# Performance work log

Hardware: AMD Instinct MI355X
Metric: run time of the kernel (lower is better)

The kernel has to match this reference:

```python
import jax, jax.numpy as jnp
import numpy as np
from jax import lax

EPS = 1e-5
MIN_SAMPLES = 4
RESHAPE = 14        # edge-map downsample factor
KEEP_FRAC = 0.1     # 1 - quantile(0.9)
KERNEL_FRAC = 0.05  # eval-mode log_kernel

SOBEL_X = jnp.array([[-1., 0., 1.], [-2., 0., 2.], [-1., 0., 1.]], jnp.float32)
SOBEL_Y = jnp.array([[-1., -2., -1.], [0., 0., 0.], [1., 2., 1.]], jnp.float32)


def _dwconv3(x, k):
    C = x.shape[1]
    kern = jnp.broadcast_to(k, (C, 1, 3, 3)).astype(x.dtype)
    return lax.conv_general_dilated(x, kern, (1, 1), 'SAME',
        feature_group_count=C, dimension_numbers=('NCHW', 'OIHW', 'NCHW'))


def _erode3(m):
    k = jnp.ones((1, 1, 3, 3), m.dtype)
    s = lax.conv_general_dilated(m, k, (1, 1), 'SAME',
        dimension_numbers=('NCHW', 'OIHW', 'NCHW'))
    return (s >= 9.0).astype(m.dtype)


def _masked_mean(x, mask, axis=-1):
    m = mask.astype(x.dtype)
    return jnp.sum(x * m, axis=axis) / jnp.maximum(jnp.sum(m, axis=axis), 1.0)


def _ssi_norm(x, mask):
    # scale-shift-invariant normalization: masked median shift, masked MAD scale
    big = jnp.where(mask, x, jnp.inf)
    srt = jnp.sort(big, axis=-1)
    n = jnp.sum(mask, axis=-1)
    idx = jnp.maximum((n - 1) // 2, 0)
    med = jnp.take_along_axis(srt, idx[..., None], axis=-1)
    med = jnp.where(n[..., None] > 0, med, 0.0)
    scale = _masked_mean(jnp.abs(x - med), mask, axis=-1)[..., None]
    return (x - med) / jnp.maximum(scale, EPS)


def _get_edge(image, vmask):
    gx = _dwconv3(image, SOBEL_X) / 8.0
    gy = _dwconv3(image, SOBEL_Y) / 8.0
    gx = jnp.sqrt(jnp.mean(gx * gx, axis=1, keepdims=True))
    gy = jnp.sqrt(jnp.mean(gy * gy, axis=1, keepdims=True))
    edges = jnp.sqrt(gx * gx + gy * gy)
    H, W = edges.shape[-2:]
    bm = jnp.zeros((H, W), edges.dtype).at[3:H - 3, 3:W - 3].set(1.0)
    return edges * bm * vmask


def _resize_bilinear(x, oh, ow):
    # torch F.interpolate bilinear, align_corners=False, no antialias
    B, C, H, W = x.shape
    def coords(o, s):
        c = jnp.clip((jnp.arange(o) + 0.5) * (s / o) - 0.5, 0.0, s - 1.0)
        i0 = jnp.floor(c).astype(jnp.int32)
        return i0, jnp.minimum(i0 + 1, s - 1), c - i0
    y0, y1, wy = coords(oh, H)
    x0, x1, wx = coords(ow, W)
    wy = wy[:, None]; wx = wx[None, :]
    g = lambda yi, xi: x[:, :, yi[:, None], xi[None, :]]
    return (g(y0, x0) * (1 - wy) * (1 - wx) + g(y0, x1) * (1 - wy) * wx
          + g(y1, x0) * wy * (1 - wx) + g(y1, x1) * wy * wx)


def _sample_edges(edges):
    B, _, H, W = edges.shape
    oh, ow = H // RESHAPE, W // RESHAPE
    e = _resize_bilinear(edges, oh, ow).reshape(B, -1)
    k = max(int(KEEP_FRAC * oh * ow), 10)
    _, idx = lax.top_k(e, k)
    return jnp.stack([(idx // ow) * RESHAPE, (idx % ow) * RESHAPE], -1).astype(jnp.int32)


def _extract_patches(x, coords, kh, kw):
    # vectorized irregular patch gather: [B,C,H,W] + [B,P,2] -> [B,P*C,kh*kw]
    B, C, H, W = x.shape
    ph, pw = kh // 2, kw // 2
    xp = jnp.pad(x, ((0, 0), (0, 0), (ph, ph), (pw, pw)))
    dy = jnp.arange(-ph, ph + 1)
    dx = jnp.arange(-pw, pw + 1)
    def one(img, y, x_):
        return img[:, (y + dy)[:, None], (x_ + dx)[None, :]]
    patches = jax.vmap(jax.vmap(one, in_axes=(None, 0, 0)))(
        xp, coords[..., 0] + ph, coords[..., 1] + pw)  # [B,P,C,kh,kw]
    return patches.reshape(B, -1, kh * kw)


def _forward(inp, tgt, mask, image, vmask):
    mask = mask.astype(bool)
    inp = inp.astype(jnp.float32)
    tgt = tgt.astype(jnp.float32)
    B, _, H, W = inp.shape
    vm = _erode3(vmask.astype(jnp.float32))
    edges = _get_edge(image.astype(jnp.float32), vm)
    coords = _sample_edges(edges)
    ks = int(KERNEL_FRAC * min(H, W))
    ks += int(ks % 2 == 0)
    # local patch branch
    pin = _extract_patches(inp, coords, ks, ks)
    ptg = _extract_patches(tgt, coords, ks, ks)
    pmk = _extract_patches(mask.astype(jnp.float32), coords, ks, ks) > 0.5
    pin = _ssi_norm(pin, pmk)
    ptg = _ssi_norm(ptg, pmk)
    err = jnp.maximum(jnp.abs(pin - ptg), EPS)
    valid = jnp.sum(pmk, axis=-1) >= MIN_SAMPLES
    ep = jnp.sqrt(jnp.maximum(_masked_mean(err, pmk, -1), EPS))  # [B,P]
    e_patch = _masked_mean(ep, valid, -1)                         # [B]
    # global image branch
    gi = _ssi_norm(inp.reshape(B, 1, H * W), mask.reshape(B, 1, H * W))
    gt = _ssi_norm(tgt.reshape(B, 1, H * W), mask.reshape(B, 1, H * W))
    gerr = jnp.maximum(jnp.abs(gi - gt), EPS)
    e_glob = jnp.sqrt(jnp.maximum(_masked_mean(gerr, mask.reshape(B, 1, H * W), -1), EPS)).squeeze(-1)
    return 0.5 * (e_patch + e_glob)  # [B]


def setup_inputs() -> dict:
    key = jax.random.key(0)
    k1, k2, k3, k4 = jax.random.split(key, 4)
    B, H, W = 32, 480, 640
    return {
        'input': jax.random.uniform(k1, (B, 1, H, W), jnp.float32, 0.1, 10.0),
        'target': jax.random.uniform(k2, (B, 1, H, W), jnp.float32, 0.1, 10.0),
        'mask': jax.random.bernoulli(k3, 0.9, (B, 1, H, W)),
        'image': jax.random.normal(k4, (B, 3, H, W), jnp.float32),
        'validity_mask': jnp.ones((B, 1, H, W), bool),
    }


def reference(input, target, mask, image, validity_mask):
    return _forward(input, target, mask, image, validity_mask)
```

## Files before the change

### kernel.cpp

```cpp
#include <hip/hip_runtime.h>
#include <math.h>

#define BB 32
#define HH 480
#define WW 640
#define HWN (HH * WW)
#define OH 34
#define OW 45
#define OHW (OH * OW)
#define KTOP 153
#define KS 25
#define PHW 12
#define PATCH (KS * KS)
#define RESHAPE_I 14
#define EPSV 1e-5f

#define TSLICE 10
#define TSW (OHW / TSLICE)

#define NSLICE 16
#define CAP 16384
#define LCAP 2048
#define CPAD 32

__device__ __forceinline__ unsigned int fkey(float f) {
  unsigned int u = __float_as_uint(f);
  return (u & 0x80000000u) ? ~u : (u | 0x80000000u);
}
__device__ __forceinline__ float fkey_inv(unsigned int k) {
  unsigned int u = (k & 0x80000000u) ? (k & 0x7FFFFFFFu) : ~k;
  return __uint_as_float(u);
}

__device__ __forceinline__ float breduce256(float v, float* red) {
  const int t = threadIdx.x;
  __syncthreads();
  red[t] = v;
  __syncthreads();
  for (int s2 = 128; s2 > 0; s2 >>= 1) {
    if (t < s2) red[t] += red[t + s2];
    __syncthreads();
  }
  float r = red[0];
  __syncthreads();
  return r;
}

__device__ __forceinline__ float2 breduce256x2(float a, float b, float* red) {
  const int t = threadIdx.x;
  __syncthreads();
  red[t] = a;
  red[256 + t] = b;
  __syncthreads();
  for (int s2 = 128; s2 > 0; s2 >>= 1) {
    if (t < s2) {
      red[t] += red[t + s2];
      red[256 + t] += red[256 + t + s2];
    }
    __syncthreads();
  }
  float2 r = make_float2(red[0], red[256]);
  __syncthreads();
  return r;
}

__device__ float edge_at(const float* __restrict__ image, const unsigned char* __restrict__ vmask,
                         int b, int y, int x) {
  if (y < 3 || y >= HH - 3 || x < 3 || x >= WW - 3) return 0.f;
  const unsigned char* vm = vmask + (size_t)b * HWN;
  #pragma unroll
  for (int dy = -1; dy <= 1; ++dy) {
    #pragma unroll
    for (int dx = -1; dx <= 1; ++dx) {
      if (!vm[(size_t)(y + dy) * WW + (x + dx)]) return 0.f;
    }
  }
  const float* img = image + (size_t)b * 3 * HWN;
  float sx2 = 0.f, sy2 = 0.f;
  #pragma unroll
  for (int c = 0; c < 3; ++c) {
    const float* p = img + (size_t)c * HWN + (size_t)y * WW + x;
    float a00 = p[-WW - 1], a01 = p[-WW], a02 = p[-WW + 1];
    float a10 = p[-1],                    a12 = p[1];
    float a20 = p[WW - 1],  a21 = p[WW],  a22 = p[WW + 1];
    float gx = (-a00 + a02 + -2.f * a10 + 2.f * a12 + -a20 + a22) / 8.f;
    float gy = (-a00 + -2.f * a01 + -a02 + a20 + 2.f * a21 + a22) / 8.f;
    sx2 += gx * gx;
    sy2 += gy * gy;
  }
  float gxm = sqrtf(sx2 / 3.f);
  float gym = sqrtf(sy2 / 3.f);
  return sqrtf(gxm * gxm + gym * gym);
}

__global__ __launch_bounds__(256) void edge_resize_kernel(const float* __restrict__ image,
                                                          const unsigned char* __restrict__ vmask,
                                                          float* __restrict__ re) {
  int id = blockIdx.x * 256 + threadIdx.x;
  if (id >= BB * OHW) return;
  int b = id / OHW;
  int rem = id % OHW;
  int oy = rem / OW, ox = rem % OW;

  const float ry = (float)((double)HH / (double)OH);
  const float rx = (float)((double)WW / (double)OW);
  float cy = fminf(fmaxf(((float)oy + 0.5f) * ry - 0.5f, 0.f), (float)(HH - 1));
  float cx = fminf(fmaxf(((float)ox + 0.5f) * rx - 0.5f, 0.f), (float)(WW - 1));
  int y0 = (int)floorf(cy);
  int x0 = (int)floorf(cx);
  int y1 = min(y0 + 1, HH - 1);
  int x1 = min(x0 + 1, WW - 1);
  float wy = cy - (float)y0;
  float wx = cx - (float)x0;

  float g00 = edge_at(image, vmask, b, y0, x0);
  float g01 = edge_at(image, vmask, b, y0, x1);
  float g10 = edge_at(image, vmask, b, y1, x0);
  float g11 = edge_at(image, vmask, b, y1, x1);
  re[id] = g00 * (1.f - wy) * (1.f - wx) + g01 * (1.f - wy) * wx +
           g10 * wy * (1.f - wx) + g11 * wy * wx;
}

__global__ __launch_bounds__(256) void topk_rank_kernel(const float* __restrict__ re,
                                                        int* __restrict__ rpart) {
  const int b = blockIdx.x / TSLICE;
  const int sl = blockIdx.x % TSLICE;
  const int t = threadIdx.x;
  __shared__ float e[OHW];
  for (int i = t; i < OHW; i += 256) e[i] = re[b * OHW + i];
  __syncthreads();

  float vi[6];
  int idx[6], cnt[6];
  #pragma unroll
  for (int q = 0; q < 6; ++q) {
    int i = t + q * 256;
    idx[q] = i;
    vi[q] = (i < OHW) ? e[i] : 0.f;
    cnt[q] = 0;
  }
  const int j0 = sl * TSW;
  for (int jj = 0; jj < TSW; ++jj) {
    int j = j0 + jj;
    float u = e[j];
    #pragma unroll
    for (int q = 0; q < 6; ++q) {
      cnt[q] += (u > vi[q]) || (u == vi[q] && j < idx[q]);
    }
  }
  int* rp = rpart + ((size_t)b * TSLICE + sl) * OHW;
  #pragma unroll
  for (int q = 0; q < 6; ++q) {
    if (idx[q] < OHW) rp[idx[q]] = cnt[q];
  }
}

__global__ __launch_bounds__(256) void topk_write_kernel(const int* __restrict__ rpart,
                                                         int* __restrict__ coords) {
  const int b = blockIdx.x;
  const int t = threadIdx.x;
  const int* rp = rpart + (size_t)b * TSLICE * OHW;
  for (int i = t; i < OHW; i += 256) {
    int rank = 0;
    #pragma unroll
    for (int sl = 0; sl < TSLICE; ++sl) rank += rp[sl * OHW + i];
    if (rank < KTOP) {
      coords[(b * KTOP + rank) * 2 + 0] = (i / OW) * RESHAPE_I;
      coords[(b * KTOP + rank) * 2 + 1] = (i % OW) * RESHAPE_I;
    }
  }
}

__global__ __launch_bounds__(256) void patch_kernel(const float* __restrict__ inp,
                                                    const float* __restrict__ tgt,
                                                    const unsigned char* __restrict__ mask,
                                                    const int* __restrict__ coords,
                                                    float* __restrict__ ep, float* __restrict__ val) {
  const int bk = blockIdx.x;
  const int b = bk / KTOP;
  const int t = threadIdx.x;
  __shared__ unsigned int hist[512];
  __shared__ unsigned int scan[512];
  __shared__ float redf[512];
  __shared__ unsigned int sh_pref[2];
  __shared__ int sh_rank[2];

  const int cy = coords[bk * 2 + 0];
  const int cx = coords[bk * 2 + 1];

  float v_in[3], v_tg[3], mk[3];
  unsigned int k_in[3], k_tg[3];
  #pragma unroll
  for (int q = 0; q < 3; ++q) {
    int i = t + q * 256;
    float mkv = 0.f, vi = 0.f, vt = 0.f;
    if (i < PATCH) {
      int dy = i / KS - PHW, dx = i % KS - PHW;
      int y = cy + dy, x = cx + dx;
      if (y >= 0 && y < HH && x >= 0 && x < WW) {
        size_t off = (size_t)b * HWN + (size_t)y * WW + x;
        if (mask[off]) mkv = 1.f;
        vi = inp[off];
        vt = tgt[off];
      }
    }
    v_in[q] = vi; v_tg[q] = vt; mk[q] = mkv;
    k_in[q] = fkey(vi); k_tg[q] = fkey(vt);
  }

  float pn = 0.f;
  #pragma unroll
  for (int q = 0; q < 3; ++q) pn += mk[q];
  float nf = breduce256(pn, redf);
  int n = (int)(nf + 0.5f);
  int r = (n > 0) ? ((n - 1) >> 1) : 0;

  if (t == 0) {
    sh_pref[0] = 0; sh_pref[1] = 0;
    sh_rank[0] = r; sh_rank[1] = r;
  }
  __syncthreads();

  #pragma unroll
  for (int p = 0; p < 4; ++p) {
    const int shift = 24 - 8 * p;
    hist[t] = 0; hist[t + 256] = 0;
    __syncthreads();
    const int r_in = sh_rank[0], r_tg = sh_rank[1];
    const unsigned int pref_in = sh_pref[0], pref_tg = sh_pref[1];
    #pragma unroll
    for (int q = 0; q < 3; ++q) {
      if (mk[q] != 0.f) {
        unsigned int k = k_in[q];
        if (p == 0 || (k >> (shift + 8)) == pref_in)
          atomicAdd(&hist[(k >> shift) & 255u], 1u);
        unsigned int k2 = k_tg[q];
        if (p == 0 || (k2 >> (shift + 8)) == pref_tg)
          atomicAdd(&hist[256 + ((k2 >> shift) & 255u)], 1u);
      }
    }
    __syncthreads();
    scan[t] = hist[t]; scan[t + 256] = hist[t + 256];
    __syncthreads();
    #pragma unroll
    for (int d = 1; d < 256; d <<= 1) {
      unsigned int a = 0, b2 = 0;
      if (t >= d) { a = scan[t - d]; b2 = scan[256 + t - d]; }
      __syncthreads();
      scan[t] += a; scan[256 + t] += b2;
      __syncthreads();
    }
    unsigned int c1 = scan[t], p1 = (t > 0) ? scan[t - 1] : 0;
    if ((unsigned int)r_in >= p1 && (unsigned int)r_in < c1) {
      sh_pref[0] = (pref_in << 8) | (unsigned int)t;
      sh_rank[0] = r_in - (int)p1;
    }
    unsigned int c2 = scan[256 + t], p2 = (t > 0) ? scan[256 + t - 1] : 0;
    if ((unsigned int)r_tg >= p2 && (unsigned int)r_tg < c2) {
      sh_pref[1] = (pref_tg << 8) | (unsigned int)t;
      sh_rank[1] = r_tg - (int)p2;
    }
    __syncthreads();
  }

  float med_i = (n > 0) ? fkey_inv(sh_pref[0]) : 0.f;
  float med_t = (n > 0) ? fkey_inv(sh_pref[1]) : 0.f;

  float pi = 0.f, pt = 0.f;
  #pragma unroll
  for (int q = 0; q < 3; ++q) {
    if (mk[q] != 0.f) {
      pi += fabsf(v_in[q] - med_i);
      pt += fabsf(v_tg[q] - med_t);
    }
  }
  float2 ss = breduce256x2(pi, pt, redf);
  float si = fmaxf(ss.x / fmaxf(nf, 1.f), EPSV);
  float st = fmaxf(ss.y / fmaxf(nf, 1.f), EPSV);

  float pe = 0.f;
  #pragma unroll
  for (int q = 0; q < 3; ++q) {
    if (mk[q] != 0.f) {
      float a = (v_in[q] - med_i) / si;
      float c = (v_tg[q] - med_t) / st;
      pe += fmaxf(fabsf(a - c), EPSV);
    }
  }
  float es = breduce256(pe, redf);
  if (t == 0) {
    ep[bk] = sqrtf(fmaxf(es / fmaxf(nf, 1.f), EPSV));
    val[bk] = (n >= 4) ? 1.f : 0.f;
  }
}

__global__ __launch_bounds__(256) void preduce_kernel(const float* __restrict__ ep,
                                                      const float* __restrict__ val,
                                                      float* __restrict__ e_patch) {
  const int b = blockIdx.x;
  const int t = threadIdx.x;
  __shared__ float red[512];
  float se = 0.f, sv = 0.f;
  for (int i = t; i < KTOP; i += 256) {
    float v = val[b * KTOP + i];
    se += ep[b * KTOP + i] * v;
    sv += v;
  }
  float2 tt = breduce256x2(se, sv, red);
  if (t == 0) e_patch[b] = tt.x / fmaxf(tt.y, 1.f);
}

__global__ __launch_bounds__(256) void gpassA_kernel(const float* __restrict__ inp,
                                                     const float* __restrict__ tgt,
                                                     const unsigned char* __restrict__ mask,
                                                     unsigned int* __restrict__ ghistA) {
  const int b = blockIdx.x / NSLICE;
  const int sl = blockIdx.x % NSLICE;
  const int t = threadIdx.x;
  __shared__ unsigned int hist[512];
  hist[t] = 0; hist[t + 256] = 0;
  __syncthreads();
  const float4* xi4 = (const float4*)(inp + (size_t)b * HWN);
  const float4* xt4 = (const float4*)(tgt + (size_t)b * HWN);
  const unsigned int* m4 = (const unsigned int*)(mask + (size_t)b * HWN);
  const int per4 = (HWN / NSLICE) / 4;
  const int s0 = sl * per4;
  for (int i = s0 + t; i < s0 + per4; i += 256) {
    unsigned int mm = m4[i];
    if (!mm) continue;
    float4 a = xi4[i], c = xt4[i];
    if (mm & 0x000000FFu) { atomicAdd(&hist[fkey(a.x) >> 24], 1u); atomicAdd(&hist[256 + (fkey(c.x) >> 24)], 1u); }
    if (mm & 0x0000FF00u) { atomicAdd(&hist[fkey(a.y) >> 24], 1u); atomicAdd(&hist[256 + (fkey(c.y) >> 24)], 1u); }
    if (mm & 0x00FF0000u) { atomicAdd(&hist[fkey(a.z) >> 24], 1u); atomicAdd(&hist[256 + (fkey(c.z) >> 24)], 1u); }
    if (mm & 0xFF000000u) { atomicAdd(&hist[fkey(a.w) >> 24], 1u); atomicAdd(&hist[256 + (fkey(c.w) >> 24)], 1u); }
  }
  __syncthreads();
  unsigned int h0 = hist[t], h1 = hist[t + 256];
  if (h0) atomicAdd(&ghistA[(b * 2 + 0) * 256 + t], h0);
  if (h1) atomicAdd(&ghistA[(b * 2 + 1) * 256 + t], h1);
}

__global__ __launch_bounds__(64) void gselA_kernel(const unsigned int* __restrict__ ghistA,
                                                   int* __restrict__ selA) {
  const int bs = blockIdx.x;
  if (threadIdx.x != 0) return;
  const unsigned int* gh = ghistA + bs * 256;
  unsigned int n = 0;
  for (int i = 0; i < 256; ++i) n += gh[i];
  int c1 = -1, r1 = 0;
  unsigned int nb = 0;
  if (n > 0) {
    unsigned int r = (n - 1) >> 1, cum = 0;
    int bin = 0;
    for (; bin < 256; ++bin) {
      unsigned int h = gh[bin];
      if (cum + h > r) break;
      cum += h;
    }
    c1 = bin; r1 = (int)(r - cum); nb = cum;
  }
  selA[bs * 4 + 0] = c1;
  selA[bs * 4 + 1] = r1;
  selA[bs * 4 + 2] = (int)n;
  selA[bs * 4 + 3] = (int)nb;
}

__global__ __launch_bounds__(256) void gpassB_kernel(const float* __restrict__ inp,
                                                     const float* __restrict__ tgt,
                                                     const unsigned char* __restrict__ mask,
                                                     const int* __restrict__ selA,
                                                     unsigned int* __restrict__ ghistB) {
  const int b = blockIdx.x / NSLICE;
  const int sl = blockIdx.x % NSLICE;
  const int t = threadIdx.x;
  __shared__ unsigned int hist[512];
  hist[t] = 0; hist[t + 256] = 0;
  __syncthreads();
  const unsigned int c1i = (unsigned int)selA[(b * 2 + 0) * 4];
  const unsigned int c1t = (unsigned int)selA[(b * 2 + 1) * 4];
  const float4* xi4 = (const float4*)(inp + (size_t)b * HWN);
  const float4* xt4 = (const float4*)(tgt + (size_t)b * HWN);
  const unsigned int* m4 = (const unsigned int*)(mask + (size_t)b * HWN);
  const int per4 = (HWN / NSLICE) / 4;
  const int s0 = sl * per4;
  for (int i = s0 + t; i < s0 + per4; i += 256) {
    unsigned int mm = m4[i];
    if (!mm) continue;
    float4 a = xi4[i], c = xt4[i];
    #define GPB(av, cv, bit) \
      if (mm & bit) { \
        unsigned int k = fkey(av); \
        if ((k >> 24) == c1i) atomicAdd(&hist[(k >> 16) & 255u], 1u); \
        unsigned int k2 = fkey(cv); \
        if ((k2 >> 24) == c1t) atomicAdd(&hist[256 + ((k2 >> 16) & 255u)], 1u); \
      }
    GPB(a.x, c.x, 0x000000FFu)
    GPB(a.y, c.y, 0x0000FF00u)
    GPB(a.z, c.z, 0x00FF0000u)
    GPB(a.w, c.w, 0xFF000000u)
    #undef GPB
  }
  __syncthreads();
  unsigned int h0 = hist[t], h1 = hist[t + 256];
  if (h0) atomicAdd(&ghistB[(b * 2 + 0) * 256 + t], h0);
  if (h1) atomicAdd(&ghistB[(b * 2 + 1) * 256 + t], h1);
}

__global__ __launch_bounds__(64) void gselB_kernel(const unsigned int* __restrict__ ghistB,
                                                   const int* __restrict__ selA,
                                                   int* __restrict__ selB) {
  const int bs = blockIdx.x;
  if (threadIdx.x != 0) return;
  const int c1 = selA[bs * 4 + 0];
  const int r1 = selA[bs * 4 + 1];
  const int n = selA[bs * 4 + 2];
  const int nb1 = selA[bs * 4 + 3];
  if (c1 < 0) {
    selB[bs * 4 + 0] = -1;
    selB[bs * 4 + 1] = 0;
    selB[bs * 4 + 2] = 0;
    selB[bs * 4 + 3] = 0;
    return;
  }
  const unsigned int* gh = ghistB + bs * 256;
  unsigned int r = (unsigned int)r1, cum = 0;
  int bin = 0;
  for (; bin < 256; ++bin) {
    unsigned int h = gh[bin];
    if (cum + h > r) break;
    cum += h;
  }
  selB[bs * 4 + 0] = (c1 << 8) | bin;
  selB[bs * 4 + 1] = (int)(r - cum);
  selB[bs * 4 + 2] = n;
  selB[bs * 4 + 3] = nb1 + (int)cum;
}

__global__ __launch_bounds__(256) void gcollect_kernel(const float* __restrict__ inp,
                                                       const float* __restrict__ tgt,
                                                       const unsigned char* __restrict__ mask,
                                                       const int* __restrict__ selB,
                                                       float* __restrict__ cand,
                                                       unsigned int* __restrict__ ccount,
                                                       float* __restrict__ sbelow,
                                                       float* __restrict__ sabove) {
  const int bs = blockIdx.x / NSLICE;
  const int sl = blockIdx.x % NSLICE;
  const int b = bs >> 1, s = bs & 1;
  const float* x = (s == 0 ? inp : tgt) + (size_t)b * HWN;
  const unsigned char* m = mask + (size_t)b * HWN;
  const int prefix = selB[bs * 4 + 0];
  __shared__ float red[512];
  __shared__ float buf[LCAP];
  __shared__ unsigned int lcnt, gbase;
  const int t = threadIdx.x;
  if (t == 0) lcnt = 0;
  __syncthreads();
  float sb = 0.f, sa = 0.f;
  if (prefix >= 0) {
    float* cd = cand + (size_t)bs * CAP;
    const float4* x4 = (const float4*)x;
    const unsigned int* m4 = (const unsigned int*)m;
    const int per4 = (HWN / NSLICE) / 4;
    const int s0 = sl * per4;
    for (int i = s0 + t; i < s0 + per4; i += 256) {
      unsigned int mm = m4[i];
      if (!mm) continue;
      float4 a = x4[i];
      #define GCOL(av, bit) \
        if (mm & bit) { \
          float v = av; \
          int pf = (int)(fkey(v) >> 16); \
          if (pf < prefix) sb += v; \
          else if (pf > prefix) sa += v; \
          else { \
            unsigned int pos = atomicAdd(&lcnt, 1u); \
            if (pos < LCAP) buf[pos] = v; \
            else { \
              unsigned int g = atomicAdd(&ccount[bs * CPAD], 1u); \
              if (g < CAP) cd[g] = v; \
            } \
          } \
        }
      GCOL(a.x, 0x000000FFu)
      GCOL(a.y, 0x0000FF00u)
      GCOL(a.z, 0x00FF0000u)
      GCOL(a.w, 0xFF000000u)
      #undef GCOL
    }
  }
  __syncthreads();
  if (prefix >= 0) {
    unsigned int c = min(lcnt, (unsigned int)LCAP);
    if (t == 0 && c > 0) gbase = atomicAdd(&ccount[bs * CPAD], c);
    __syncthreads();
    if (c > 0) {
      float* cd = cand + (size_t)bs * CAP;
      unsigned int base = gbase;
      for (unsigned int i = t; i < c; i += 256) {
        unsigned int pos = base + i;
        if (pos < CAP) cd[pos] = buf[i];
      }
    }
  }
  float2 ts = breduce256x2(sb, sa, red);
  if (t == 0) {
    atomicAdd(&sbelow[bs], ts.x);
    atomicAdd(&sabove[bs], ts.y);
  }
}

__global__ __launch_bounds__(256) void gfinal_kernel(const float* __restrict__ cand,
                                                     const unsigned int* __restrict__ ccount,
                                                     const int* __restrict__ selB,
                                                     const float* __restrict__ sbelow,
                                                     const float* __restrict__ sabove,
                                                     float* __restrict__ gstats,
                                                     float* __restrict__ nvals) {
  const int bs = blockIdx.x;
  const int t = threadIdx.x;
  const int prefix = selB[bs * 4 + 0];
  const int r2 = selB[bs * 4 + 1];
  const int n = selB[bs * 4 + 2];
  const int nbelow = selB[bs * 4 + 3];
  __shared__ unsigned int hist[256];
  __shared__ float red[256];
  __shared__ int sh_bin1, sh_r3;
  const float* cd = cand + (size_t)bs * CAP;
  int c = (int)min(ccount[bs * CPAD], (unsigned int)CAP);
  if (prefix < 0) {
    if (t == 0) {
      gstats[bs * 2 + 0] = 0.f;
      gstats[bs * 2 + 1] = 0.f;
      if ((bs & 1) == 0) nvals[bs >> 1] = 0.f;
    }
    return;
  }

  hist[t] = 0;
  __syncthreads();
  for (int i = t; i < c; i += 256)
    atomicAdd(&hist[(fkey(cd[i]) >> 8) & 255u], 1u);
  __syncthreads();
  if (t == 0) {
    unsigned int rr = (unsigned int)r2, cum = 0;
    int bin = 0;
    for (; bin < 256; ++bin) {
      unsigned int h = hist[bin];
      if (cum + h > rr) break;
      cum += h;
    }
    sh_bin1 = bin;
    sh_r3 = (int)(rr - cum);
  }
  __syncthreads();
  const int bin1 = sh_bin1;
  const int r3 = sh_r3;

  hist[t] = 0;
  __syncthreads();
  for (int i = t; i < c; i += 256) {
    unsigned int key = fkey(cd[i]);
    if (((key >> 8) & 255u) == (unsigned int)bin1)
      atomicAdd(&hist[key & 255u], 1u);
  }
  __syncthreads();
  __shared__ float sh_med;
  if (t == 0) {
    unsigned int rr = (unsigned int)r3, cum = 0;
    int bin = 0;
    for (; bin < 256; ++bin) {
      unsigned int h = hist[bin];
      if (cum + h > rr) break;
      cum += h;
    }
    unsigned int key = ((unsigned int)prefix << 16) |
                       ((unsigned int)bin1 << 8) | (unsigned int)bin;
    sh_med = fkey_inv(key);
  }
  __syncthreads();
  const float med = sh_med;

  float ps = 0.f;
  for (int i = t; i < c; i += 256) ps += fabsf(cd[i] - med);
  float scand = breduce256(ps, red);
  if (t == 0) {
    float nb = (float)nbelow;
    float na = (float)(n - nbelow - c);
    float num = (nb * med - sbelow[bs]) + (sabove[bs] - na * med) + scand;
    gstats[bs * 2 + 0] = med;
    gstats[bs * 2 + 1] = num / fmaxf((float)n, 1.f);
    if ((bs & 1) == 0) nvals[bs >> 1] = (float)n;
  }
}

__global__ __launch_bounds__(256) void gerr_kernel(const float* __restrict__ inp,
                                                   const float* __restrict__ tgt,
                                                   const unsigned char* __restrict__ mask,
                                                   const float* __restrict__ gstats,
                                                   float* __restrict__ gacc) {
  const int b = blockIdx.x / NSLICE;
  const int sl = blockIdx.x % NSLICE;
  __shared__ float red[256];
  const int t = threadIdx.x;
  const float med_i = gstats[(b * 2 + 0) * 2 + 0];
  const float sc_i = fmaxf(gstats[(b * 2 + 0) * 2 + 1], EPSV);
  const float med_t = gstats[(b * 2 + 1) * 2 + 0];
  const float sc_t = fmaxf(gstats[(b * 2 + 1) * 2 + 1], EPSV);
  const float ri = 1.f / sc_i, rt = 1.f / sc_t;
  const float4* xi4 = (const float4*)(inp + (size_t)b * HWN);
  const float4* xt4 = (const float4*)(tgt + (size_t)b * HWN);
  const unsigned int* m4 = (const unsigned int*)(mask + (size_t)b * HWN);
  const int per4 = (HWN / NSLICE) / 4;
  const int s0 = sl * per4;
  float part = 0.f;
  for (int i = s0 + t; i < s0 + per4; i += 256) {
    unsigned int mm = m4[i];
    if (!mm) continue;
    float4 a = xi4[i], c = xt4[i];
    if (mm & 0x000000FFu) part += fmaxf(fabsf((a.x - med_i) * ri - (c.x - med_t) * rt), EPSV);
    if (mm & 0x0000FF00u) part += fmaxf(fabsf((a.y - med_i) * ri - (c.y - med_t) * rt), EPSV);
    if (mm & 0x00FF0000u) part += fmaxf(fabsf((a.z - med_i) * ri - (c.z - med_t) * rt), EPSV);
    if (mm & 0xFF000000u) part += fmaxf(fabsf((a.w - med_i) * ri - (c.w - med_t) * rt), EPSV);
  }
  float tp = breduce256(part, red);
  if (t == 0) atomicAdd(&gacc[b], tp);
}

__global__ __launch_bounds__(64) void final_kernel(const float* __restrict__ gacc,
                                                   const float* __restrict__ nvals,
                                                   const float* __restrict__ e_patch,
                                                   float* __restrict__ out) {
  const int b = threadIdx.x;
  if (b < BB) {
    float n = nvals[b];
    float eg = sqrtf(fmaxf(gacc[b] / fmaxf(n, 1.f), EPSV));
    out[b] = 0.5f * (e_patch[b] + eg);
  }
}

extern "C" void kernel_launch(void* const* d_in, const int* in_sizes, int n_in,
                              void* d_out, int out_size, void* d_ws, size_t ws_size,
                              hipStream_t stream) {
  const float* inp = (const float*)d_in[0];
  const float* tgt = (const float*)d_in[1];
  const unsigned char* mask = (const unsigned char*)d_in[2];
  const float* image = (const float*)d_in[3];
  const unsigned char* vmask = (const unsigned char*)d_in[4];
  float* out = (float*)d_out;

  float* ws = (float*)d_ws;
  float* re = ws;
  int* coords = (int*)(ws + 48960);
  float* ep = ws + 48960 + 9792;
  float* val = ep + 4896;
  float* e_patch = val + 4896;
  float* gstats = e_patch + 32;
  float* nvals = gstats + 128;
  int* selA = (int*)(nvals + 32);
  int* selB = selA + 256;
  float* cand = (float*)(selB + 256);
  unsigned int* ghistA = (unsigned int*)(cand + (size_t)64 * CAP);
  unsigned int* ghistB = ghistA + 64 * 256;
  unsigned int* ccount = ghistB + 64 * 256;
  float* sbelow = (float*)(ccount + 64 * CPAD);
  float* sabove = sbelow + 64;
  float* gacc = sabove + 64;
  size_t zero_bytes = ((size_t)64 * 256 * 2 + 64 * CPAD + 64 + 64 + 32) * 4;
  hipMemsetAsync(ghistA, 0, zero_bytes, stream);

  int* rpart = (int*)cand;

  edge_resize_kernel<<<(BB * OHW + 255) / 256, 256, 0, stream>>>(image, vmask, re);
  topk_rank_kernel<<<BB * TSLICE, 256, 0, stream>>>(re, rpart);
  topk_write_kernel<<<BB, 256, 0, stream>>>(rpart, coords);
  patch_kernel<<<BB * KTOP, 256, 0, stream>>>(inp, tgt, mask, coords, ep, val);
  preduce_kernel<<<BB, 256, 0, stream>>>(ep, val, e_patch);
  gpassA_kernel<<<BB * NSLICE, 256, 0, stream>>>(inp, tgt, mask, ghistA);
  gselA_kernel<<<BB * 2, 64, 0, stream>>>(ghistA, selA);
  gpassB_kernel<<<BB * NSLICE, 256, 0, stream>>>(inp, tgt, mask, selA, ghistB);
  gselB_kernel<<<BB * 2, 64, 0, stream>>>(ghistB, selA, selB);
  gcollect_kernel<<<BB * 2 * NSLICE, 256, 0, stream>>>(inp, tgt, mask, selB, cand, ccount, sbelow, sabove);
  gfinal_kernel<<<BB * 2, 256, 0, stream>>>(cand, ccount, selB, sbelow, sabove, gstats, nvals);
  gerr_kernel<<<BB * NSLICE, 256, 0, stream>>>(inp, tgt, mask, gstats, gacc);
  final_kernel<<<1, 64, 0, stream>>>(gacc, nvals, e_patch, out);
}
```

Baseline: 451.4 us.

## Use single-wavefront patch median, split edge corners across lanes, double global slices

The patch kernel now runs as one 64-lane wavefront per patch. It replaces the shared-memory block reductions and the 256-step barrier scan with wave shuffles and a per-lane 4-bin local scan. This removes many __syncthreads, at the cost of each thread holding 10 elements. The edge-resize kernel gives each bilinear corner to its own lane and combines the four with shuffles, which raises parallelism for the Sobel work. The three global streaming passes use 32 slices per image instead of 16 to put more blocks in flight.

```diff
diff --git a/kernel.cpp b/kernel.cpp
--- a/kernel.cpp
+++ b/kernel.cpp
@@ -18,6 +18,7 @@
 #define TSLICE 10
 #define TSW (OHW / TSLICE)
 
+#define PSLICE 32
 #define NSLICE 16
 #define CAP 16384
 #define LCAP 2048
@@ -96,10 +97,11 @@
 __global__ __launch_bounds__(256) void edge_resize_kernel(const float* __restrict__ image,
                                                           const unsigned char* __restrict__ vmask,
                                                           float* __restrict__ re) {
-  int id = blockIdx.x * 256 + threadIdx.x;
-  if (id >= BB * OHW) return;
-  int b = id / OHW;
-  int rem = id % OHW;
+  int gid = blockIdx.x * 256 + threadIdx.x;
+  int corner = gid & 3;
+  int cell = gid >> 2;
+  int b = cell / OHW;
+  int rem = cell % OHW;
   int oy = rem / OW, ox = rem % OW;
 
   const float ry = (float)((double)HH / (double)OH);
@@ -113,12 +115,13 @@
   float wy = cy - (float)y0;
   float wx = cx - (float)x0;
 
-  float g00 = edge_at(image, vmask, b, y0, x0);
-  float g01 = edge_at(image, vmask, b, y0, x1);
-  float g10 = edge_at(image, vmask, b, y1, x0);
-  float g11 = edge_at(image, vmask, b, y1, x1);
-  re[id] = g00 * (1.f - wy) * (1.f - wx) + g01 * (1.f - wy) * wx +
-           g10 * wy * (1.f - wx) + g11 * wy * wx;
+  int yy = (corner & 2) ? y1 : y0;
+  int xx = (corner & 1) ? x1 : x0;
+  float w = ((corner & 2) ? wy : 1.f - wy) * ((corner & 1) ? wx : 1.f - wx);
+  float g = edge_at(image, vmask, b, yy, xx) * w;
+  g += __shfl_xor(g, 1, 64);
+  g += __shfl_xor(g, 2, 64);
+  if (corner == 0) re[cell] = g;
 }
 
 __global__ __launch_bounds__(256) void topk_rank_kernel(const float* __restrict__ re,
@@ -171,49 +174,48 @@
   }
 }
 
-__global__ __launch_bounds__(256) void patch_kernel(const float* __restrict__ inp,
-                                                    const float* __restrict__ tgt,
-                                                    const unsigned char* __restrict__ mask,
-                                                    const int* __restrict__ coords,
-                                                    float* __restrict__ ep, float* __restrict__ val) {
+__global__ __launch_bounds__(64) void patch_kernel(const float* __restrict__ inp,
+                                                   const float* __restrict__ tgt,
+                                                   const unsigned char* __restrict__ mask,
+                                                   const int* __restrict__ coords,
+                                                   float* __restrict__ ep, float* __restrict__ val) {
   const int bk = blockIdx.x;
   const int b = bk / KTOP;
   const int t = threadIdx.x;
   __shared__ unsigned int hist[512];
-  __shared__ unsigned int scan[512];
-  __shared__ float redf[512];
   __shared__ unsigned int sh_pref[2];
   __shared__ int sh_rank[2];
 
   const int cy = coords[bk * 2 + 0];
   const int cx = coords[bk * 2 + 1];
 
-  float v_in[3], v_tg[3], mk[3];
-  unsigned int k_in[3], k_tg[3];
-  #pragma unroll
-  for (int q = 0; q < 3; ++q) {
-    int i = t + q * 256;
-    float mkv = 0.f, vi = 0.f, vt = 0.f;
+  float v_in[10], v_tg[10];
+  unsigned int k_in[10], k_tg[10];
+  unsigned int mbits = 0;
+  #pragma unroll
+  for (int q = 0; q < 10; ++q) {
+    int i = t + q * 64;
+    float vi = 0.f, vt = 0.f;
     if (i < PATCH) {
       int dy = i / KS - PHW, dx = i % KS - PHW;
       int y = cy + dy, x = cx + dx;
       if (y >= 0 && y < HH && x >= 0 && x < WW) {
         size_t off = (size_t)b * HWN + (size_t)y * WW + x;
-        if (mask[off]) mkv = 1.f;
+        if (mask[off]) mbits |= (1u << q);
         vi = inp[off];
         vt = tgt[off];
       }
     }
-    v_in[q] = vi; v_tg[q] = vt; mk[q] = mkv;
+    v_in[q] = vi; v_tg[q] = vt;
     k_in[q] = fkey(vi); k_tg[q] = fkey(vt);
   }
 
-  float pn = 0.f;
-  #pragma unroll
-  for (int q = 0; q < 3; ++q) pn += mk[q];
-  float nf = breduce256(pn, redf);
-  int n = (int)(nf + 0.5f);
-  int r = (n > 0) ? ((n - 1) >> 1) : 0;
+  int pn = __popc(mbits);
+  #pragma unroll
+  for (int d = 32; d > 0; d >>= 1) pn += __shfl_xor(pn, d, 64);
+  const int n = pn;
+  const float nf = (float)n;
+  const int r = (n > 0) ? ((n - 1) >> 1) : 0;
 
   if (t == 0) {
     sh_pref[0] = 0; sh_pref[1] = 0;
@@ -224,13 +226,14 @@
   #pragma unroll
   for (int p = 0; p < 4; ++p) {
     const int shift = 24 - 8 * p;
-    hist[t] = 0; hist[t + 256] = 0;
+    #pragma unroll
+    for (int j = 0; j < 8; ++j) hist[t + 64 * j] = 0;
     __syncthreads();
     const int r_in = sh_rank[0], r_tg = sh_rank[1];
     const unsigned int pref_in = sh_pref[0], pref_tg = sh_pref[1];
     #pragma unroll
-    for (int q = 0; q < 3; ++q) {
-      if (mk[q] != 0.f) {
+    for (int q = 0; q < 10; ++q) {
+      if (mbits & (1u << q)) {
         unsigned int k = k_in[q];
         if (p == 0 || (k >> (shift + 8)) == pref_in)
           atomicAdd(&hist[(k >> shift) & 255u], 1u);
@@ -240,56 +243,74 @@
       }
     }
     __syncthreads();
-    scan[t] = hist[t]; scan[t + 256] = hist[t + 256];
+    {
+      unsigned int a0 = hist[t * 4 + 0], a1 = hist[t * 4 + 1];
+      unsigned int a2 = hist[t * 4 + 2], a3 = hist[t * 4 + 3];
+      unsigned int b0 = hist[256 + t * 4 + 0], b1 = hist[256 + t * 4 + 1];
+      unsigned int b2 = hist[256 + t * 4 + 2], b3 = hist[256 + t * 4 + 3];
+      unsigned int sa0 = a0, sa1 = sa0 + a1, sa2 = sa1 + a2, sa3 = sa2 + a3;
+      unsigned int sb0 = b0, sb1 = sb0 + b1, sb2 = sb1 + b2, sb3 = sb2 + b3;
+      unsigned int ta = sa3, tb = sb3;
+      #pragma unroll
+      for (int d = 1; d < 64; d <<= 1) {
+        unsigned int ua = (unsigned int)__shfl_up((int)ta, d, 64);
+        unsigned int ub = (unsigned int)__shfl_up((int)tb, d, 64);
+        if (t >= d) { ta += ua; tb += ub; }
+      }
+      unsigned int exa = ta - sa3, exb = tb - sb3;
+      unsigned int rra = (unsigned int)r_in, rrb = (unsigned int)r_tg;
+      unsigned int pa[4] = {exa, exa + sa0, exa + sa1, exa + sa2};
+      unsigned int ca[4] = {exa + sa0, exa + sa1, exa + sa2, exa + sa3};
+      unsigned int pb[4] = {exb, exb + sb0, exb + sb1, exb + sb2};
+      unsigned int cb[4] = {exb + sb0, exb + sb1, exb + sb2, exb + sb3};
+      #pragma unroll
+      for (int j = 0; j < 4; ++j) {
+        if (rra >= pa[j] && rra < ca[j]) {
+          sh_pref[0] = (pref_in << 8) | (unsigned int)(t * 4 + j);
+          sh_rank[0] = (int)(rra - pa[j]);
+        }
+        if (rrb >= pb[j] && rrb < cb[j]) {
+          sh_pref[1] = (pref_tg << 8) | (unsigned int)(t * 4 + j);
+          sh_rank[1] = (int)(rrb - pb[j]);
+        }
+      }
+    }
     __syncthreads();
-    #pragma unroll
-    for (int d = 1; d < 256; d <<= 1) {
-      unsigned int a = 0, b2 = 0;
-      if (t >= d) { a = scan[t - d]; b2 = scan[256 + t - d]; }
-      __syncthreads();
-      scan[t] += a; scan[256 + t] += b2;
-      __syncthreads();
-    }
-    unsigned int c1 = scan[t], p1 = (t > 0) ? scan[t - 1] : 0;
-    if ((unsigned int)r_in >= p1 && (unsigned int)r_in < c1) {
-      sh_pref[0] = (pref_in << 8) | (unsigned int)t;
-      sh_rank[0] = r_in - (int)p1;
-    }
-    unsigned int c2 = scan[256 + t], p2 = (t > 0) ? scan[256 + t - 1] : 0;
-    if ((unsigned int)r_tg >= p2 && (unsigned int)r_tg < c2) {
-      sh_pref[1] = (pref_tg << 8) | (unsigned int)t;
-      sh_rank[1] = r_tg - (int)p2;
-    }
-    __syncthreads();
-  }
-
-  float med_i = (n > 0) ? fkey_inv(sh_pref[0]) : 0.f;
-  float med_t = (n > 0) ? fkey_inv(sh_pref[1]) : 0.f;
+  }
+
+  const float med_i = (n > 0) ? fkey_inv(sh_pref[0]) : 0.f;
+  const float med_t = (n > 0) ? fkey_inv(sh_pref[1]) : 0.f;
 
   float pi = 0.f, pt = 0.f;
   #pragma unroll
-  for (int q = 0; q < 3; ++q) {
-    if (mk[q] != 0.f) {
+  for (int q = 0; q < 10; ++q) {
+    if (mbits & (1u << q)) {
       pi += fabsf(v_in[q] - med_i);
       pt += fabsf(v_tg[q] - med_t);
     }
   }
-  float2 ss = breduce256x2(pi, pt, redf);
-  float si = fmaxf(ss.x / fmaxf(nf, 1.f), EPSV);
-  float st = fmaxf(ss.y / fmaxf(nf, 1.f), EPSV);
+  #pragma unroll
+  for (int d = 32; d > 0; d >>= 1) {
+    pi += __shfl_xor(pi, d, 64);
+    pt += __shfl_xor(pt, d, 64);
+  }
+  const float si = fmaxf(pi / fmaxf(nf, 1.f), EPSV);
+  const float st = fmaxf(pt / fmaxf(nf, 1.f), EPSV);
 
   float pe = 0.f;
   #pragma unroll
-  for (int q = 0; q < 3; ++q) {
-    if (mk[q] != 0.f) {
+  for (int q = 0; q < 10; ++q) {
+    if (mbits & (1u << q)) {
       float a = (v_in[q] - med_i) / si;
       float c = (v_tg[q] - med_t) / st;
       pe += fmaxf(fabsf(a - c), EPSV);
     }
   }
-  float es = breduce256(pe, redf);
+  #pragma unroll
+  for (int d = 32; d > 0; d >>= 1) pe += __shfl_xor(pe, d, 64);
+
   if (t == 0) {
-    ep[bk] = sqrtf(fmaxf(es / fmaxf(nf, 1.f), EPSV));
+    ep[bk] = sqrtf(fmaxf(pe / fmaxf(nf, 1.f), EPSV));
     val[bk] = (n >= 4) ? 1.f : 0.f;
   }
 }
@@ -314,8 +335,8 @@
                                                      const float* __restrict__ tgt,
                                                      const unsigned char* __restrict__ mask,
                                                      unsigned int* __restrict__ ghistA) {
-  const int b = blockIdx.x / NSLICE;
-  const int sl = blockIdx.x % NSLICE;
+  const int b = blockIdx.x / PSLICE;
+  const int sl = blockIdx.x % PSLICE;
   const int t = threadIdx.x;
   __shared__ unsigned int hist[512];
   hist[t] = 0; hist[t + 256] = 0;
@@ -323,7 +344,7 @@
   const float4* xi4 = (const float4*)(inp + (size_t)b * HWN);
   const float4* xt4 = (const float4*)(tgt + (size_t)b * HWN);
   const unsigned int* m4 = (const unsigned int*)(mask + (size_t)b * HWN);
-  const int per4 = (HWN / NSLICE) / 4;
+  const int per4 = (HWN / PSLICE) / 4;
   const int s0 = sl * per4;
   for (int i = s0 + t; i < s0 + per4; i += 256) {
     unsigned int mm = m4[i];
@@ -370,8 +391,8 @@
                                                      const unsigned char* __restrict__ mask,
                                                      const int* __restrict__ selA,
                                                      unsigned int* __restrict__ ghistB) {
-  const int b = blockIdx.x / NSLICE;
-  const int sl = blockIdx.x % NSLICE;
+  const int b = blockIdx.x / PSLICE;
+  const int sl = blockIdx.x % PSLICE;
   const int t = threadIdx.x;
   __shared__ unsigned int hist[512];
   hist[t] = 0; hist[t + 256] = 0;
@@ -381,7 +402,7 @@
   const float4* xi4 = (const float4*)(inp + (size_t)b * HWN);
   const float4* xt4 = (const float4*)(tgt + (size_t)b * HWN);
   const unsigned int* m4 = (const unsigned int*)(mask + (size_t)b * HWN);
-  const int per4 = (HWN / NSLICE) / 4;
+  const int per4 = (HWN / PSLICE) / 4;
   const int s0 = sl * per4;
   for (int i = s0 + t; i < s0 + per4; i += 256) {
     unsigned int mm = m4[i];
@@ -599,8 +620,8 @@
                                                    const unsigned char* __restrict__ mask,
                                                    const float* __restrict__ gstats,
                                                    float* __restrict__ gacc) {
-  const int b = blockIdx.x / NSLICE;
-  const int sl = blockIdx.x % NSLICE;
+  const int b = blockIdx.x / PSLICE;
+  const int sl = blockIdx.x % PSLICE;
   __shared__ float red[256];
   const int t = threadIdx.x;
   const float med_i = gstats[(b * 2 + 0) * 2 + 0];
@@ -611,7 +632,7 @@
   const float4* xi4 = (const float4*)(inp + (size_t)b * HWN);
   const float4* xt4 = (const float4*)(tgt + (size_t)b * HWN);
   const unsigned int* m4 = (const unsigned int*)(mask + (size_t)b * HWN);
-  const int per4 = (HWN / NSLICE) / 4;
+  const int per4 = (HWN / PSLICE) / 4;
   const int s0 = sl * per4;
   float part = 0.f;
   for (int i = s0 + t; i < s0 + per4; i += 256) {
@@ -671,17 +692,17 @@
 
   int* rpart = (int*)cand;
 
-  edge_resize_kernel<<<(BB * OHW + 255) / 256, 256, 0, stream>>>(image, vmask, re);
+  edge_resize_kernel<<<(BB * OHW * 4) / 256, 256, 0, stream>>>(image, vmask, re);
   topk_rank_kernel<<<BB * TSLICE, 256, 0, stream>>>(re, rpart);
   topk_write_kernel<<<BB, 256, 0, stream>>>(rpart, coords);
-  patch_kernel<<<BB * KTOP, 256, 0, stream>>>(inp, tgt, mask, coords, ep, val);
+  patch_kernel<<<BB * KTOP, 64, 0, stream>>>(inp, tgt, mask, coords, ep, val);
   preduce_kernel<<<BB, 256, 0, stream>>>(ep, val, e_patch);
-  gpassA_kernel<<<BB * NSLICE, 256, 0, stream>>>(inp, tgt, mask, ghistA);
+  gpassA_kernel<<<BB * PSLICE, 256, 0, stream>>>(inp, tgt, mask, ghistA);
   gselA_kernel<<<BB * 2, 64, 0, stream>>>(ghistA, selA);
-  gpassB_kernel<<<BB * NSLICE, 256, 0, stream>>>(inp, tgt, mask, selA, ghistB);
+  gpassB_kernel<<<BB * PSLICE, 256, 0, stream>>>(inp, tgt, mask, selA, ghistB);
   gselB_kernel<<<BB * 2, 64, 0, stream>>>(ghistB, selA, selB);
   gcollect_kernel<<<BB * 2 * NSLICE, 256, 0, stream>>>(inp, tgt, mask, selB, cand, ccount, sbelow, sabove);
   gfinal_kernel<<<BB * 2, 256, 0, stream>>>(cand, ccount, selB, sbelow, sabove, gstats, nvals);
-  gerr_kernel<<<BB * NSLICE, 256, 0, stream>>>(inp, tgt, mask, gstats, gacc);
+  gerr_kernel<<<BB * PSLICE, 256, 0, stream>>>(inp, tgt, mask, gstats, gacc);
   final_kernel<<<1, 64, 0, stream>>>(gacc, nvals, e_patch, out);
 }
```

Result: faster. 427.0 us (-5.4%).
